# Kernel tuning notes

Measured on AMD Instinct MI355X. Metric: run time of the kernel, lower is better.

Reference implementation:

```python
import jax, jax.numpy as jnp
import numpy as np

B, T, D_IN, D_OUT = 16, 2048, 2048, 2048
N_ADAPTERS, RANK = 8, 16


def setup_inputs() -> dict:
    key = jax.random.key(0)
    k_x, k_w, k_a, k_b, k_s, k_idx = jax.random.split(key, 6)
    x = jax.random.normal(k_x, (B, T, D_IN), dtype=jnp.float32)
    # frozen base weight (nn.Linear stores W as (d_out, d_in)); bias=False
    W = jax.random.normal(k_w, (D_OUT, D_IN), dtype=jnp.float32) * (1.0 / np.sqrt(D_IN))
    # stacked adapter bank: A[a] is (r, d_in), Bm[a] is (d_out, r)
    A = jax.random.normal(k_a, (N_ADAPTERS, RANK, D_IN), dtype=jnp.float32) * 0.02
    Bm = jax.random.normal(k_b, (N_ADAPTERS, D_OUT, RANK), dtype=jnp.float32) * 0.02
    scalings = jnp.ones((N_ADAPTERS,), dtype=jnp.float32)  # alpha / r, pre-merged
    adapter_idx = jax.random.randint(k_idx, (B,), 0, N_ADAPTERS, dtype=jnp.int32)
    return {"x": x, "W": W, "A": A, "Bm": Bm, "scalings": scalings,
            "adapter_idx": adapter_idx}


def reference(x, W, A, Bm, scalings, adapter_idx):
    # base path: H = x @ W^T   -> (B, T, d_out)
    H = jnp.einsum("btd,od->bto", x, W)
    # per-request adapter gather (replaces the Python loop over adapter groups)
    A_b = A[adapter_idx]          # (B, r, d_in)
    B_b = Bm[adapter_idx]         # (B, d_out, r)
    s_b = scalings[adapter_idx]   # (B,)
    # low-rank delta: (x @ A^T) @ B^T, done per request, fully batched
    xa = jnp.einsum("btd,brd->btr", x, A_b)        # (B, T, r)
    delta = jnp.einsum("btr,bor->bto", xa, B_b)    # (B, T, d_out)
    # original computes delta under torch.no_grad() with detached A/B
    delta = jax.lax.stop_gradient(delta * s_b[:, None, None])
    return H + delta
```

## Files before the change

kernel.cpp:

```cpp
#include <hip/hip_runtime.h>
#include <stdint.h>

typedef unsigned short u16;
typedef __attribute__((ext_vector_type(4))) short s16x4;
typedef __attribute__((ext_vector_type(8))) short short8;
typedef __attribute__((ext_vector_type(4))) float f32x4;
typedef __attribute__((ext_vector_type(16))) float f32x16;

static __device__ __forceinline__ u16 f2bf(float f) {
    union { float f; uint32_t u; } c; c.f = f;
    uint32_t u = c.u;
    u += 0x7FFFu + ((u >> 16) & 1u);
    return (u16)(u >> 16);
}

#define D_IN   2048
#define D_OUT  2048
#define MTOT   32768
#define BK     64
#define NTM    32

__device__ __forceinline__ void gload16(const u16* g, u16* l) {
    __builtin_amdgcn_global_load_lds(
        (const __attribute__((address_space(1))) void*)g,
        (__attribute__((address_space(3))) void*)l, 16, 0, 0);
}

__global__ __launch_bounds__(256) void k_prep(
    const float* __restrict__ W, const float* __restrict__ A, const float* __restrict__ Bm,
    u16* __restrict__ Wb, u16* __restrict__ Ap, u16* __restrict__ Bp)
{
    const int b = blockIdx.x, tid = threadIdx.x;
    if (b < 2048) {
        int i = (b * 256 + tid) * 8;
        const float4* p = (const float4*)(W + i);
        float4 v0 = p[0], v1 = p[1];
        short8 o;
        o[0]=f2bf(v0.x); o[1]=f2bf(v0.y); o[2]=f2bf(v0.z); o[3]=f2bf(v0.w);
        o[4]=f2bf(v1.x); o[5]=f2bf(v1.y); o[6]=f2bf(v1.z); o[7]=f2bf(v1.w);
        *(short8*)(Wb + i) = o;
    } else if (b < 6144) {
        int i = (b - 2048) * 256 + tid;
        int d = i & 2047, r = (i >> 11) & 63, a = i >> 17;
        Ap[i] = (r < 16) ? f2bf(A[(((a << 4) + r) << 11) + d]) : (u16)0;
    } else {
        int i = (b - 6144) * 256 + tid;
        int j = i & 63, n = (i >> 6) & 2047, a = i >> 17;
        Bp[i] = (j < 16) ? f2bf(Bm[((((a << 11) + n)) << 4) + j]) : (u16)0;
    }
}

__global__ __launch_bounds__(256) void k_cast_x_xa(
    const float* __restrict__ x, const u16* __restrict__ Ap,
    const float* __restrict__ scal, const int* __restrict__ aidx,
    u16* __restrict__ xb, u16* __restrict__ xa)
{
    __shared__ __align__(16) u16 Xs[128 * BK];
    __shared__ __align__(16) u16 Ps[64 * BK];
    const int tid = threadIdx.x, lane = tid & 63, wid = tid >> 6;
    const int m0 = blockIdx.x << 7;
    const int a = aidx[m0 >> 11];
    const float s = scal[a];
    const int wr = wid >> 1, wc = wid & 1;
    const int arow = (wr << 6) + (lane & 15);
    const int brow = (wc << 5) + (lane & 15);
    const int scol = ((lane & 7) ^ (lane >> 3)) << 3;

    f32x4 acc[4][2];
    #pragma unroll
    for (int i = 0; i < 4; ++i) { acc[i][0] = 0.f; acc[i][1] = 0.f; }

    const int xrow_l = tid >> 4;
    const int xcol   = (tid & 15) << 2;
    const int wslot  = (tid & 15) >> 1;
    const int wsub   = (tid & 1) << 2;

    const u16* apg = Ap + ((size_t)a << 17);
    const u16* gP[2]; u16* lP[2];
    #pragma unroll
    for (int it = 0; it < 2; ++it) {
        const int chunk = (wid << 1) + it;
        const int row = (chunk << 3) + (lane >> 3);
        gP[it] = apg + ((size_t)row << 11) + scol;
        lP[it] = Ps + (chunk << 9) + (lane << 3);
    }

    for (int kt = 0; kt < NTM; ++kt) {
        const int k0 = kt << 6;
        float4 xv[8];
        #pragma unroll
        for (int r = 0; r < 8; ++r)
            xv[r] = *(const float4*)(x + ((size_t)(m0 + (r << 4) + xrow_l) << 11) + k0 + xcol);
        #pragma unroll
        for (int r = 0; r < 8; ++r) {
            const int row = (r << 4) + xrow_l;
            s16x4 c4;
            c4[0]=f2bf(xv[r].x); c4[1]=f2bf(xv[r].y); c4[2]=f2bf(xv[r].z); c4[3]=f2bf(xv[r].w);
            *(s16x4*)(Xs + (row << 6) + ((wslot ^ (row & 7)) << 3) + wsub) = c4;
            *(s16x4*)(xb + ((size_t)(m0 + row) << 11) + k0 + xcol) = c4;
        }
        gload16(gP[0] + k0, lP[0]);
        gload16(gP[1] + k0, lP[1]);
        asm volatile("s_waitcnt vmcnt(0)" ::: "memory");
        __syncthreads();
        #pragma unroll
        for (int kk = 0; kk < 2; ++kk) {
            const int sl = ((kk << 2) + (lane >> 4)) ^ (lane & 7);
            short8 af[4], bv[2];
            #pragma unroll
            for (int mi = 0; mi < 4; ++mi)
                af[mi] = *(const short8*)(Xs + ((arow + mi * 16) << 6) + (sl << 3));
            #pragma unroll
            for (int ni = 0; ni < 2; ++ni)
                bv[ni] = *(const short8*)(Ps + ((brow + ni * 16) << 6) + (sl << 3));
            #pragma unroll
            for (int mi = 0; mi < 4; ++mi)
                #pragma unroll
                for (int ni = 0; ni < 2; ++ni)
                    acc[mi][ni] = __builtin_amdgcn_mfma_f32_16x16x32_bf16(af[mi], bv[ni], acc[mi][ni], 0, 0, 0);
        }
        __syncthreads();
    }

    #pragma unroll
    for (int mi = 0; mi < 4; ++mi) {
        #pragma unroll
        for (int ni = 0; ni < 2; ++ni) {
            const int cc = (wc << 5) + ni * 16 + (lane & 15);
            #pragma unroll
            for (int rr = 0; rr < 4; ++rr) {
                const int mm = m0 + (wr << 6) + mi * 16 + ((lane >> 4) << 2) + rr;
                xa[((size_t)mm << 6) + cc] = f2bf(acc[mi][ni][rr] * s);
            }
        }
    }
}

__global__ __launch_bounds__(512, 2) void k_gemm(
    const u16* __restrict__ xb, const u16* __restrict__ Wb,
    const u16* __restrict__ xa, const u16* __restrict__ Bp,
    const int* __restrict__ aidx, float* __restrict__ out)
{
    __shared__ __align__(16) u16 LDS[2 * 32768];
    const int tid = threadIdx.x, lane = tid & 63, wid = tid >> 6;

    const int newbid = (blockIdx.x & 7) * 128 + (blockIdx.x >> 3);
    const int bm = newbid >> 3, bn = newbid & 7;
    const int m0 = bm << 8, n0 = bn << 8;
    const int wr = wid >> 2, wc = wid & 3;
    const int a = aidx[m0 >> 11];

    f32x16 acc[4][2];
    #pragma unroll
    for (int i = 0; i < 4; ++i)
        #pragma unroll
        for (int j = 0; j < 2; ++j)
            #pragma unroll
            for (int r = 0; r < 16; ++r) acc[i][j][r] = 0.0f;

    const int sc  = ((tid & 7) ^ ((tid >> 3) & 7)) << 3;
    const int srw = tid >> 3;
    const u16 *pA[2], *pB[2], *tA[2], *tB[2];
    #pragma unroll
    for (int h = 0; h < 2; ++h) {
        pA[h] = xb + ((size_t)(m0 + (h << 7) + srw) << 11) + sc;
        pB[h] = Wb + ((size_t)(n0 + (h << 7) + srw) << 11) + sc;
        tA[h] = xa + ((size_t)(m0 + (h << 7) + srw) << 6) + sc;
        tB[h] = Bp + ((((size_t)a << 11) + n0 + (h << 7) + srw) << 6) + sc;
    }
    const int dbase = tid << 3;

    #define SAm(tt, h, c1) do { const u16* g_ = pA[h] + ((tt) << 6);               \
        u16* d_ = &LDS[((c1) << 15) + ((h) << 13) + dbase];                         \
        gload16(g_, d_); gload16(g_ + (64 << 11), d_ + 4096); } while (0)
    #define SAt(h, c1) do { const u16* g_ = tA[h];                                  \
        u16* d_ = &LDS[((c1) << 15) + ((h) << 13) + dbase];                         \
        gload16(g_, d_); gload16(g_ + (64 << 6), d_ + 4096); } while (0)
    #define SBm(tt, h, c1) do { const u16* g_ = pB[h] + ((tt) << 6);               \
        u16* d_ = &LDS[((c1) << 15) + 16384 + ((h) << 13) + dbase];                 \
        gload16(g_, d_); gload16(g_ + (64 << 11), d_ + 4096); } while (0)
    #define SBt(h, c1) do { const u16* g_ = tB[h];                                  \
        u16* d_ = &LDS[((c1) << 15) + 16384 + ((h) << 13) + dbase];                 \
        gload16(g_, d_); gload16(g_ + (64 << 6), d_ + 4096); } while (0)

    const int l31 = lane & 31, h5 = lane >> 5, lw7 = lane & 7;
    int sl[4];
    #pragma unroll
    for (int ks = 0; ks < 4; ++ks) sl[ks] = ((((ks << 1) | h5) ^ lw7) << 3);
    const int abase = ((wr << 7) + l31) << 6;
    const int bbase = 16384 + (((wc << 6) + l31) << 6);

    short8 af[2][4], bv[2][4];

    #define RDA2(c_, mlo) do { _Pragma("unroll")                                    \
        for (int mi = 0; mi < 2; ++mi) _Pragma("unroll")                            \
        for (int ks = 0; ks < 4; ++ks)                                              \
            af[mi][ks] = *(const short8*)&LDS[((c_) << 15) + abase +                \
                                              (((mlo) + mi) << 11) + sl[ks]]; } while (0)
    #define RDB1(c_, nb) do { _Pragma("unroll")                                     \
        for (int ks = 0; ks < 4; ++ks)                                              \
            bv[nb][ks] = *(const short8*)&LDS[((c_) << 15) + bbase +                \
                                              ((nb) << 11) + sl[ks]]; } while (0)

    #define BAR  __builtin_amdgcn_s_barrier()
    #define LGK0 do { asm volatile("s_waitcnt lgkmcnt(0)" ::: "memory");            \
                      __builtin_amdgcn_sched_barrier(0); } while (0)

    #define MM2(mlo, nb) do { __builtin_amdgcn_s_setprio(1); _Pragma("unroll")      \
        for (int ks = 0; ks < 4; ++ks) _Pragma("unroll")                            \
        for (int mi = 0; mi < 2; ++mi)                                              \
            acc[(mlo) + mi][nb] = __builtin_amdgcn_mfma_f32_32x32x16_bf16(          \
                af[mi][ks], bv[nb][ks], acc[(mlo) + mi][nb], 0, 0, 0);              \
        __builtin_amdgcn_s_setprio(0); } while (0)

    SAm(0, 0, 0); SAm(0, 1, 0); SBm(0, 0, 0); SBm(0, 1, 0); SBm(1, 0, 1); SBm(1, 1, 1);
    asm volatile("s_waitcnt vmcnt(4)" ::: "memory");
    BAR;

    for (int t = 0; t <= NTM; ++t) {
        const int c = t & 1;
        RDB1(c, 0); RDA2(c, 0);
        if (t + 1 < NTM) SAm(t + 1, 0, c ^ 1); else if (t + 1 == NTM) SAt(0, c ^ 1);
        BAR; LGK0; MM2(0, 0); BAR;
        RDB1(c, 1);
        if (t + 1 < NTM) SAm(t + 1, 1, c ^ 1); else if (t + 1 == NTM) SAt(1, c ^ 1);
        BAR; LGK0; MM2(0, 1); BAR;
        RDA2(c, 2);
        if (t + 2 < NTM) SBm(t + 2, 0, c); else if (t + 2 == NTM) SBt(0, c);
        BAR; LGK0; MM2(2, 0); BAR;
        if (t + 2 < NTM) SBm(t + 2, 1, c); else if (t + 2 == NTM) SBt(1, c);
        BAR; MM2(2, 1);
        if (t < NTM - 1)       asm volatile("s_waitcnt vmcnt(4)" ::: "memory");
        else if (t == NTM - 1) asm volatile("s_waitcnt vmcnt(0)" ::: "memory");
        BAR;
    }

    #undef MM2
    #undef LGK0
    #undef BAR
    #undef RDB1
    #undef RDA2
    #undef SBt
    #undef SBm
    #undef SAt
    #undef SAm

    #pragma unroll
    for (int mb = 0; mb < 4; ++mb) {
        #pragma unroll
        for (int nb = 0; nb < 2; ++nb) {
            const int nn = n0 + (wc << 6) + (nb << 5) + l31;
            #pragma unroll
            for (int r = 0; r < 16; ++r) {
                const int row = (r & 3) + ((r >> 2) << 3) + (h5 << 2);
                const int mm = m0 + (wr << 7) + (mb << 5) + row;
                out[((size_t)mm << 11) + nn] = acc[mb][nb][r];
            }
        }
    }
}

extern "C" void kernel_launch(void* const* d_in, const int* in_sizes, int n_in,
                              void* d_out, int out_size, void* d_ws, size_t ws_size,
                              hipStream_t stream) {
    const float* x  = (const float*)d_in[0];
    const float* W  = (const float*)d_in[1];
    const float* A  = (const float*)d_in[2];
    const float* Bm = (const float*)d_in[3];
    const float* sc = (const float*)d_in[4];
    const int* aidx = (const int*)d_in[5];
    float* out = (float*)d_out;

    char* ws = (char*)d_ws;
    u16* xb = (u16*)(ws);
    u16* Wb = (u16*)(ws + 134217728);
    u16* Ap = (u16*)(ws + 134217728 + 8388608);
    u16* Bp = (u16*)(ws + 134217728 + 8388608 + 2097152);
    u16* xa = (u16*)(ws + 134217728 + 8388608 + 2097152 + 2097152);

    hipLaunchKernelGGL(k_prep,      dim3(10240), dim3(256), 0, stream, W, A, Bm, Wb, Ap, Bp);
    hipLaunchKernelGGL(k_cast_x_xa, dim3(256),   dim3(256), 0, stream, x, Ap, sc, aidx, xb, xa);
    hipLaunchKernelGGL(k_gemm,      dim3(1024),  dim3(512), 0, stream, xb, Wb, xa, Bp, aidx, out);
}
```

Baseline: 430.8 us.

## Switch to 16x16x32 MFMA with register double-buffered LDS fragment pipeline

Replaces the 32x32x16 MFMA tiles with 16x16x32 MFMAs in 8x4 f32x4 accumulators and restructures the main loop. Fragments for the next compute chunk are read from LDS while the current MFMAs run, using partial lgkmcnt waits. The global-to-LDS schedule changes to load a whole K-stage ahead with one vmcnt(0) per iteration. The goal is to hide LDS read latency behind matrix math and cut the number of barriers per iteration. The cost is more fragment registers and a less deep global prefetch, since the B operand was previously loaded two stages ahead.

```diff
diff --git a/kernel.cpp b/kernel.cpp
--- a/kernel.cpp
+++ b/kernel.cpp
@@ -5,7 +5,6 @@
 typedef __attribute__((ext_vector_type(4))) short s16x4;
 typedef __attribute__((ext_vector_type(8))) short short8;
 typedef __attribute__((ext_vector_type(4))) float f32x4;
-typedef __attribute__((ext_vector_type(16))) float f32x16;
 
 static __device__ __forceinline__ u16 f2bf(float f) {
     union { float f; uint32_t u; } c; c.f = f;
@@ -150,13 +149,11 @@
     const int wr = wid >> 2, wc = wid & 3;
     const int a = aidx[m0 >> 11];
 
-    f32x16 acc[4][2];
-    #pragma unroll
-    for (int i = 0; i < 4; ++i)
-        #pragma unroll
-        for (int j = 0; j < 2; ++j)
-            #pragma unroll
-            for (int r = 0; r < 16; ++r) acc[i][j][r] = 0.0f;
+    f32x4 acc[8][4];
+    #pragma unroll
+    for (int i = 0; i < 8; ++i)
+        #pragma unroll
+        for (int j = 0; j < 4; ++j) acc[i][j] = 0.0f;
 
     const int sc  = ((tid & 7) ^ ((tid >> 3) & 7)) << 3;
     const int srw = tid >> 3;
@@ -182,79 +179,85 @@
     #define SBt(h, c1) do { const u16* g_ = tB[h];                                  \
         u16* d_ = &LDS[((c1) << 15) + 16384 + ((h) << 13) + dbase];                 \
         gload16(g_, d_); gload16(g_ + (64 << 6), d_ + 4096); } while (0)
-
-    const int l31 = lane & 31, h5 = lane >> 5, lw7 = lane & 7;
-    int sl[4];
-    #pragma unroll
-    for (int ks = 0; ks < 4; ++ks) sl[ks] = ((((ks << 1) | h5) ^ lw7) << 3);
-    const int abase = ((wr << 7) + l31) << 6;
-    const int bbase = 16384 + (((wc << 6) + l31) << 6);
-
-    short8 af[2][4], bv[2][4];
-
-    #define RDA2(c_, mlo) do { _Pragma("unroll")                                    \
-        for (int mi = 0; mi < 2; ++mi) _Pragma("unroll")                            \
-        for (int ks = 0; ks < 4; ++ks)                                              \
-            af[mi][ks] = *(const short8*)&LDS[((c_) << 15) + abase +                \
-                                              (((mlo) + mi) << 11) + sl[ks]]; } while (0)
-    #define RDB1(c_, nb) do { _Pragma("unroll")                                     \
-        for (int ks = 0; ks < 4; ++ks)                                              \
-            bv[nb][ks] = *(const short8*)&LDS[((c_) << 15) + bbase +                \
-                                              ((nb) << 11) + sl[ks]]; } while (0)
-
-    #define BAR  __builtin_amdgcn_s_barrier()
-    #define LGK0 do { asm volatile("s_waitcnt lgkmcnt(0)" ::: "memory");            \
-                      __builtin_amdgcn_sched_barrier(0); } while (0)
-
-    #define MM2(mlo, nb) do { __builtin_amdgcn_s_setprio(1); _Pragma("unroll")      \
-        for (int ks = 0; ks < 4; ++ks) _Pragma("unroll")                            \
-        for (int mi = 0; mi < 2; ++mi)                                              \
-            acc[(mlo) + mi][nb] = __builtin_amdgcn_mfma_f32_32x32x16_bf16(          \
-                af[mi][ks], bv[nb][ks], acc[(mlo) + mi][nb], 0, 0, 0);              \
+    #define STAGE_MAIN(tt, c1) do { SAm(tt,0,c1); SAm(tt,1,c1); SBm(tt,0,c1); SBm(tt,1,c1); } while (0)
+    #define STAGE_TAIL(c1)     do { SAt(0,c1);    SAt(1,c1);    SBt(0,c1);    SBt(1,c1);    } while (0)
+
+    const int sl0 = (((lane >> 4)    ) ^ (lane & 7)) << 3;
+    const int sl1 = (((lane >> 4) + 4) ^ (lane & 7)) << 3;
+    const int aRowBase = (wr << 7) + (lane & 15);
+    const int bRowBase = (wc << 6) + (lane & 15);
+
+    short8 afX[4], afY[4], bvP[4], bvQ[4];
+
+    #define RAF(dst, c_, mh, slx) do { _Pragma("unroll")                            \
+        for (int mi = 0; mi < 4; ++mi) {                                            \
+            const int row = aRowBase + ((mh) << 6) + (mi << 4);                     \
+            dst[mi] = *(const short8*)&LDS[((c_) << 15) + (row << 6) + (slx)];      \
+        } } while (0)
+    #define RBV(dst, c_, slx) do { _Pragma("unroll")                                \
+        for (int ni = 0; ni < 4; ++ni) {                                            \
+            const int row = bRowBase + (ni << 4);                                   \
+            dst[ni] = *(const short8*)&LDS[((c_) << 15) + 16384 + (row << 6) + (slx)]; \
+        } } while (0)
+
+    #define BAR __builtin_amdgcn_s_barrier()
+    #define LGK(n) do { asm volatile("s_waitcnt lgkmcnt(" #n ")" ::: "memory");     \
+                        __builtin_amdgcn_sched_barrier(0); } while (0)
+
+    #define MMC(afS, bvS, mh) do { __builtin_amdgcn_s_setprio(1); _Pragma("unroll") \
+        for (int mi = 0; mi < 4; ++mi) _Pragma("unroll")                            \
+        for (int ni = 0; ni < 4; ++ni)                                              \
+            acc[(mh) * 4 + mi][ni] = __builtin_amdgcn_mfma_f32_16x16x32_bf16(       \
+                afS[mi], bvS[ni], acc[(mh) * 4 + mi][ni], 0, 0, 0);                 \
         __builtin_amdgcn_s_setprio(0); } while (0)
 
-    SAm(0, 0, 0); SAm(0, 1, 0); SBm(0, 0, 0); SBm(0, 1, 0); SBm(1, 0, 1); SBm(1, 1, 1);
-    asm volatile("s_waitcnt vmcnt(4)" ::: "memory");
+    STAGE_MAIN(0, 0);
+    asm volatile("s_waitcnt vmcnt(0)" ::: "memory");
     BAR;
+    RAF(afX, 0, 0, sl0); RBV(bvP, 0, sl0);
 
     for (int t = 0; t <= NTM; ++t) {
-        const int c = t & 1;
-        RDB1(c, 0); RDA2(c, 0);
-        if (t + 1 < NTM) SAm(t + 1, 0, c ^ 1); else if (t + 1 == NTM) SAt(0, c ^ 1);
-        BAR; LGK0; MM2(0, 0); BAR;
-        RDB1(c, 1);
-        if (t + 1 < NTM) SAm(t + 1, 1, c ^ 1); else if (t + 1 == NTM) SAt(1, c ^ 1);
-        BAR; LGK0; MM2(0, 1); BAR;
-        RDA2(c, 2);
-        if (t + 2 < NTM) SBm(t + 2, 0, c); else if (t + 2 == NTM) SBt(0, c);
-        BAR; LGK0; MM2(2, 0); BAR;
-        if (t + 2 < NTM) SBm(t + 2, 1, c); else if (t + 2 == NTM) SBt(1, c);
-        BAR; MM2(2, 1);
-        if (t < NTM - 1)       asm volatile("s_waitcnt vmcnt(4)" ::: "memory");
-        else if (t == NTM - 1) asm volatile("s_waitcnt vmcnt(0)" ::: "memory");
+        const int c = t & 1, cn = c ^ 1;
+        RAF(afY, c, 1, sl0);
+        if (t + 1 < NTM)       STAGE_MAIN(t + 1, cn);
+        else if (t + 1 == NTM) STAGE_TAIL(cn);
+        LGK(4);
+        MMC(afX, bvP, 0);
+        RAF(afX, c, 0, sl1); RBV(bvQ, c, sl1);
+        LGK(8);
+        MMC(afY, bvP, 1);
+        RAF(afY, c, 1, sl1);
+        LGK(4);
+        MMC(afX, bvQ, 0);
+        if (t < NTM) asm volatile("s_waitcnt vmcnt(0)" ::: "memory");
         BAR;
-    }
-
-    #undef MM2
-    #undef LGK0
+        if (t < NTM) { RAF(afX, cn, 0, sl0); RBV(bvP, cn, sl0); LGK(8); }
+        else         { LGK(0); }
+        MMC(afY, bvQ, 1);
+        BAR;
+    }
+
+    #undef MMC
+    #undef LGK
     #undef BAR
-    #undef RDB1
-    #undef RDA2
+    #undef RBV
+    #undef RAF
+    #undef STAGE_TAIL
+    #undef STAGE_MAIN
     #undef SBt
     #undef SBm
     #undef SAt
     #undef SAm
 
     #pragma unroll
-    for (int mb = 0; mb < 4; ++mb) {
-        #pragma unroll
-        for (int nb = 0; nb < 2; ++nb) {
-            const int nn = n0 + (wc << 6) + (nb << 5) + l31;
-            #pragma unroll
-            for (int r = 0; r < 16; ++r) {
-                const int row = (r & 3) + ((r >> 2) << 3) + (h5 << 2);
-                const int mm = m0 + (wr << 7) + (mb << 5) + row;
-                out[((size_t)mm << 11) + nn] = acc[mb][nb][r];
+    for (int mi = 0; mi < 8; ++mi) {
+        #pragma unroll
+        for (int ni = 0; ni < 4; ++ni) {
+            const int nn = n0 + (wc << 6) + ni * 16 + (lane & 15);
+            #pragma unroll
+            for (int r = 0; r < 4; ++r) {
+                const int mm = m0 + (wr << 7) + mi * 16 + ((lane >> 4) << 2) + r;
+                out[((size_t)mm << 11) + nn] = acc[mi][ni][r];
             }
         }
     }
```

Result: faster. 399.6 us (-7.2%).
